# Performance work log

Hardware: AMD Instinct MI355X
Metric: run time of the kernel (lower is better)

The kernel has to match this reference:

```python
import jax, jax.numpy as jnp
import numpy as np

N_HEADS = 16


def setup_inputs() -> dict:
    key = jax.random.key(0)
    k1, k2, k3 = jax.random.split(key, 3)
    B, T, C = 4, 2048, 1024
    x = jax.random.normal(k1, (B, T, C), dtype=jnp.float32)
    # torch nn.Linear weights are (out_features, in_features); y = x @ W.T
    w_in = jax.random.normal(k2, (3 * C, C), dtype=jnp.float32) * 0.02
    w_out = jax.random.normal(k3, (C, C), dtype=jnp.float32) * 0.02
    return {"x": x, "w_in": w_in, "w_out": w_out}


def reference(x, w_in, w_out):
    B, T, C = x.shape
    H = N_HEADS
    hd = C // H

    qkv = x @ w_in.T                      # [B, T, 3C]
    q, k, v = jnp.split(qkv, 3, axis=2)   # each [B, T, C]

    def heads(t):
        return t.reshape(B, T, H, hd).transpose(0, 2, 1, 3)  # [B, H, T, hd]

    q, k, v = heads(q), heads(k), heads(v)

    scale = 1.0 / jnp.sqrt(jnp.float32(hd))
    scores = jnp.einsum('bhqd,bhkd->bhqk', q, k) * scale      # [B, H, T, T]
    causal = jnp.tril(jnp.ones((T, T), dtype=bool))
    scores = jnp.where(causal, scores, -jnp.inf)
    attn = jax.nn.softmax(scores, axis=-1)
    y = jnp.einsum('bhqk,bhkd->bhqd', attn, v)                # [B, H, T, hd]
    y = y.transpose(0, 2, 1, 3).reshape(B, T, C)
    return y @ w_out.T
```

## Files before the change

kernel.cpp:

```cpp
#include <hip/hip_runtime.h>
#include <stdint.h>

#define BB 4
#define TT 2048
#define CC 1024
#define HH 16
#define HD 64
#define C3 3072
#define MM (BB*TT)

typedef __bf16 bf16_t;
typedef bf16_t bf16x8 __attribute__((ext_vector_type(8)));
typedef float f32x4 __attribute__((ext_vector_type(4)));
typedef unsigned short u16;
typedef u16 u16x8 __attribute__((ext_vector_type(8)));
typedef uint32_t u32;

static __device__ __forceinline__ u16 f2bf(float f){
  u32 u = __builtin_bit_cast(u32, f);
  u32 r = (u + 0x7fffu + ((u >> 16) & 1u)) >> 16;
  return (u16)r;
}

static __device__ __forceinline__ f32x4 mfma16(bf16x8 a, bf16x8 b, f32x4 c){
  return __builtin_amdgcn_mfma_f32_16x16x32_bf16(a, b, c, 0, 0, 0);
}

typedef __attribute__((address_space(1))) void* gas_t;
typedef __attribute__((address_space(3))) void* las_t;
static __device__ __forceinline__ void gload16(const void* g, void* l){
  __builtin_amdgcn_global_load_lds((gas_t)g, (las_t)l, 16, 0, 0);
}

__global__ __launch_bounds__(256) void cvt_all(const float* __restrict__ x,
                                               const float* __restrict__ wi,
                                               const float* __restrict__ wo,
                                               u16* __restrict__ out){
  const int n1 = MM*CC/8, n2 = C3*CC/8, n3 = CC*CC/8;
  const int total = n1 + n2 + n3;
  int stride = gridDim.x * blockDim.x;
  for (int i = blockIdx.x * blockDim.x + threadIdx.x; i < total; i += stride){
    const float* src; int k;
    if (i < n1){ src = x; k = i; }
    else if (i < n1 + n2){ src = wi; k = i - n1; }
    else { src = wo; k = i - n1 - n2; }
    const float4* p = (const float4*)src + (size_t)k * 2;
    float4 a = p[0], b = p[1];
    u16x8 o;
    o[0]=f2bf(a.x); o[1]=f2bf(a.y); o[2]=f2bf(a.z); o[3]=f2bf(a.w);
    o[4]=f2bf(b.x); o[5]=f2bf(b.y); o[6]=f2bf(b.z); o[7]=f2bf(b.w);
    *((u16x8*)out + i) = o;
  }
}

template<int OUTBF>
__global__ __launch_bounds__(256) void gemm_bt(const u16* __restrict__ A,
                                               const u16* __restrict__ Bm,
                                               void* __restrict__ Cp,
                                               int M, int N, int K,
                                               int nbx, int cpx){
  __shared__ u16 As[128*64];
  __shared__ u16 Bs[128*64];
  const int bid = blockIdx.x;
  const int nb = (bid & 7) * cpx + (bid >> 3);
  const int by = nb / nbx, bx = nb - by * nbx;
  const int tid  = threadIdx.x;
  const int lane = tid & 63;
  const int w    = tid >> 6;
  const int m0   = by * 128;
  const int n0   = bx * 128;
  const int wm   = (w >> 1) * 64;
  const int wn   = (w & 1) * 64;
  const int lr   = lane & 15;
  const int lg4  = lane >> 4;

  f32x4 acc[4][4] = {};

  const int rq  = tid >> 3;
  const int c8s = ((tid & 7) ^ (rq & 7)) * 8;
  const u16* gA = A  + (size_t)(m0 + rq) * K + c8s;
  const u16* gB = Bm + (size_t)(n0 + rq) * K + c8s;
  char* lA = (char*)As + tid*16;
  char* lB = (char*)Bs + tid*16;

  for (int k0 = 0; k0 < K; k0 += 64){
    #pragma unroll
    for (int q = 0; q < 4; q++){
      gload16(gA + (size_t)(q*32)*K + k0, lA + q*4096);
      gload16(gB + (size_t)(q*32)*K + k0, lB + q*4096);
    }
    __syncthreads();
    #pragma unroll
    for (int kk = 0; kk < 2; kk++){
      bf16x8 af[4], bfr[4];
      #pragma unroll
      for (int m = 0; m < 4; m++){
        int row = wm + m*16 + lr;
        int slot = ((kk<<2) | lg4) ^ (row & 7);
        af[m] = *(const bf16x8*)((const char*)As + row*128 + slot*16);
      }
      #pragma unroll
      for (int n = 0; n < 4; n++){
        int row = wn + n*16 + lr;
        int slot = ((kk<<2) | lg4) ^ (row & 7);
        bfr[n] = *(const bf16x8*)((const char*)Bs + row*128 + slot*16);
      }
      #pragma unroll
      for (int m = 0; m < 4; m++)
        #pragma unroll
        for (int n = 0; n < 4; n++)
          acc[m][n] = mfma16(af[m], bfr[n], acc[m][n]);
    }
    __syncthreads();
  }

  const int cr = lg4 * 4;
  #pragma unroll
  for (int m = 0; m < 4; m++)
    #pragma unroll
    for (int n = 0; n < 4; n++)
      #pragma unroll
      for (int j = 0; j < 4; j++){
        size_t row = (size_t)(m0 + wm + m*16 + cr + j);
        size_t col = (size_t)(n0 + wn + n*16 + lr);
        if (OUTBF) ((u16*)Cp)[row*(size_t)N + col] = f2bf(acc[m][n][j]);
        else       ((float*)Cp)[row*(size_t)N + col] = acc[m][n][j];
      }
}

__global__ __launch_bounds__(256, 3) void attn_fwd(const u16* __restrict__ qkv,
                                                   u16* __restrict__ y){
  __shared__ u16 Kl[2][64*72];
  __shared__ u16 Vt[2][64*72];
  const int bid = blockIdx.x;
  const int tq = bid >> 6;
  const int h = bid & 15, b = (bid >> 4) & 3;
  const int tid = threadIdx.x, lane = tid & 63, w = tid >> 6;
  const int lr = lane & 15, lg = lane >> 4;
  const size_t base = (size_t)b * TT * C3;
  const int qA = tq*64 + w*16;
  const int qB = (31-tq)*64 + w*16;
  const float SC = 0.18033688011112042f;

  bf16x8 qf[2][2];
  {
    const u16* qp0 = qkv + base + (size_t)(qA + lr) * C3 + h*HD;
    qf[0][0] = *(const bf16x8*)(qp0 + lg*8);
    qf[0][1] = *(const bf16x8*)(qp0 + 32 + lg*8);
    const u16* qp1 = qkv + base + (size_t)(qB + lr) * C3 + h*HD;
    qf[1][0] = *(const bf16x8*)(qp1 + lg*8);
    qf[1][1] = *(const bf16x8*)(qp1 + 32 + lg*8);
    #pragma unroll
    for (int m = 0; m < 2; m++)
      #pragma unroll
      for (int i = 0; i < 2; i++)
        #pragma unroll
        for (int e = 0; e < 8; e++)
          qf[m][i][e] = (bf16_t)((float)qf[m][i][e] * SC);
  }

  const int rK = tid >> 3, cK = tid & 7;
  const int rp = tid & 15;
  const int dc = (tid >> 4) & 7;
  const int hf = tid >> 7;
  const u16* gK = qkv + base + (size_t)rK * C3 + CC + h*HD + cK*8;
  const u16* gV = qkv + base + (size_t)(2*rp + 32*hf) * C3 + 2*CC + h*HD + dc*8;

  const int kkey = ((rK >> 3) & 1) << 5;
  const int kw0 = rK*72 + ((cK*8) ^ kkey);
  const int kw1 = (rK+32)*72 + ((cK*8) ^ kkey);
  const int vw  = 2*rp + 32*hf;

  const int rdx = ((lr >> 2) & 1) << 5;
  const int rbase = 8*(lr >> 2) + (lr & 3);

  u16x8 kreg[2], vreg[2];
  kreg[0] = *(const u16x8*)(gK);
  kreg[1] = *(const u16x8*)(gK + (size_t)32*C3);
  vreg[0] = *(const u16x8*)(gV);
  vreg[1] = *(const u16x8*)(gV + C3);

  f32x4 o[2][4] = {};
  float mj[2] = {-1e30f, -1e30f};
  float lj[2] = {0.f, 0.f};

  const int ktmax = 31 - tq;
  for (int kt = 0; kt <= ktmax; kt++){
    const int cb = kt & 1;
    u16* KL = Kl[cb];
    u16* VT = Vt[cb];
    *(u16x8*)&KL[kw0] = kreg[0];
    *(u16x8*)&KL[kw1] = kreg[1];
    #pragma unroll
    for (int e = 0; e < 8; e++){
      u32 pk = (u32)vreg[0][e] | ((u32)vreg[1][e] << 16);
      *(u32*)&VT[(dc*8+e)*72 + vw] = pk;
    }
    __syncthreads();

    if (kt < ktmax){
      const u16* gk2 = gK + (size_t)(kt+1)*64*C3;
      const u16* gv2 = gV + (size_t)(kt+1)*64*C3;
      kreg[0] = *(const u16x8*)(gk2);
      kreg[1] = *(const u16x8*)(gk2 + (size_t)32*C3);
      vreg[0] = *(const u16x8*)(gv2);
      vreg[1] = *(const u16x8*)(gv2 + C3);
    }

    const bool m0act = (kt <= tq);

    #pragma unroll
    for (int m = 1; m >= 0; m--){
      if (m == 0 && !m0act) continue;

      f32x4 s[4] = {};
      __builtin_amdgcn_s_setprio(1);
      #pragma unroll
      for (int n = 0; n < 4; n++){
        const int rho = 32*(n>>1) + 4*(n&1) + rbase;
        bf16x8 kb0 = *(const bf16x8*)&KL[rho*72 + ((     lg*8) ^ rdx)];
        bf16x8 kb1 = *(const bf16x8*)&KL[rho*72 + ((32 + lg*8) ^ rdx)];
        s[n] = mfma16(kb0, qf[m][0], s[n]);
        s[n] = mfma16(kb1, qf[m][1], s[n]);
      }
      __builtin_amdgcn_s_setprio(0);

      const int qrow = (m ? qB : qA) + lr;
      const bool dm = (kt == (m ? ktmax : tq));
      if (dm){
        #pragma unroll
        for (int n = 0; n < 4; n++)
          #pragma unroll
          for (int j = 0; j < 4; j++)
            if (kt*64 + 32*(n>>1) + 8*lg + 4*(n&1) + j > qrow)
              s[n][j] = -1e30f;
      }
      float tm = s[0][0];
      #pragma unroll
      for (int n = 0; n < 4; n++)
        #pragma unroll
        for (int j = 0; j < 4; j++) tm = fmaxf(tm, s[n][j]);
      tm = fmaxf(tm, __shfl_xor(tm, 16, 64));
      tm = fmaxf(tm, __shfl_xor(tm, 32, 64));
      float mo = mj[m];
      if (!__all(tm <= mo + 4.0f)){
        float mn = fmaxf(mo, tm);
        float al = __builtin_amdgcn_exp2f(mo - mn);
        mj[m] = mn;
        lj[m] *= al;
        float a0 = __shfl(al, lg*4+0, 16);
        float a1 = __shfl(al, lg*4+1, 16);
        float a2 = __shfl(al, lg*4+2, 16);
        float a3 = __shfl(al, lg*4+3, 16);
        #pragma unroll
        for (int n = 0; n < 4; n++){
          o[m][n][0] *= a0; o[m][n][1] *= a1;
          o[m][n][2] *= a2; o[m][n][3] *= a3;
        }
      }
      float mm = mj[m];
      float ps = 0.f;
      bf16x8 pa, pb;
      #pragma unroll
      for (int n = 0; n < 4; n++){
        float p0 = __builtin_amdgcn_exp2f(s[n][0] - mm);
        float p1 = __builtin_amdgcn_exp2f(s[n][1] - mm);
        float p2 = __builtin_amdgcn_exp2f(s[n][2] - mm);
        float p3 = __builtin_amdgcn_exp2f(s[n][3] - mm);
        ps += (p0 + p1) + (p2 + p3);
        if (n == 0){ pa[0]=(bf16_t)p0; pa[1]=(bf16_t)p1; pa[2]=(bf16_t)p2; pa[3]=(bf16_t)p3; }
        if (n == 1){ pa[4]=(bf16_t)p0; pa[5]=(bf16_t)p1; pa[6]=(bf16_t)p2; pa[7]=(bf16_t)p3; }
        if (n == 2){ pb[0]=(bf16_t)p0; pb[1]=(bf16_t)p1; pb[2]=(bf16_t)p2; pb[3]=(bf16_t)p3; }
        if (n == 3){ pb[4]=(bf16_t)p0; pb[5]=(bf16_t)p1; pb[6]=(bf16_t)p2; pb[7]=(bf16_t)p3; }
      }
      ps += __shfl_xor(ps, 16, 64);
      ps += __shfl_xor(ps, 32, 64);
      lj[m] += ps;

      __builtin_amdgcn_s_setprio(1);
      #pragma unroll
      for (int n = 0; n < 4; n++){
        bf16x8 vb0 = *(const bf16x8*)&VT[(n*16+lr)*72 +      lg*8];
        bf16x8 vb1 = *(const bf16x8*)&VT[(n*16+lr)*72 + 32 + lg*8];
        o[m][n] = mfma16(pa, vb0, o[m][n]);
        o[m][n] = mfma16(pb, vb1, o[m][n]);
      }
      __builtin_amdgcn_s_setprio(0);
      __builtin_amdgcn_sched_barrier(0);
    }
  }

  #pragma unroll
  for (int m = 0; m < 2; m++){
    float inv = 1.0f / lj[m];
    float i0 = __shfl(inv, lg*4+0, 16);
    float i1 = __shfl(inv, lg*4+1, 16);
    float i2 = __shfl(inv, lg*4+2, 16);
    float i3 = __shfl(inv, lg*4+3, 16);
    const int qb = (m ? qB : qA);
    #pragma unroll
    for (int j = 0; j < 4; j++){
      float ij = (j==0) ? i0 : (j==1) ? i1 : (j==2) ? i2 : i3;
      size_t row = (size_t)b*TT + qb + lg*4 + j;
      #pragma unroll
      for (int n = 0; n < 4; n++)
        y[row*CC + h*HD + n*16 + lr] = f2bf(o[m][n][j] * ij);
    }
  }
}

extern "C" void kernel_launch(void* const* d_in, const int* in_sizes, int n_in,
                              void* d_out, int out_size, void* d_ws, size_t ws_size,
                              hipStream_t stream){
  const float* x     = (const float*)d_in[0];
  const float* w_in  = (const float*)d_in[1];
  const float* w_out = (const float*)d_in[2];
  float* out = (float*)d_out;

  u16* xb   = (u16*)d_ws;
  u16* wib  = xb  + (size_t)MM * CC;
  u16* wob  = wib + (size_t)C3 * CC;
  u16* qkvb = wob + (size_t)CC * CC;
  u16* yb   = xb;

  cvt_all<<<2048, 256, 0, stream>>>(x, w_in, w_out, xb);

  gemm_bt<1><<<1536, 256, 0, stream>>>(xb, wib, (void*)qkvb, MM, C3, CC, 24, 192);
  attn_fwd<<<1024, 256, 0, stream>>>(qkvb, yb);
  gemm_bt<0><<<512, 256, 0, stream>>>(yb, wob, (void*)out, MM, CC, CC, 8, 64);
}
```

Before: 166.9 us.

## Hoist V fragment loads across both query tiles and swizzle V^T smem

Loads the V^T fragments from shared memory once per key tile into registers and reuses them for both query row groups, instead of reloading them for each group. Adds an XOR swizzle on the V^T column index to reduce LDS bank conflicts. Also reshapes the max and sum reductions into trees, removes the sched_barrier, and lowers the launch-bounds occupancy hint from 3 to 2 to make room for the extra registers. The cost is higher register pressure and possibly fewer resident waves per CU.

```diff
diff --git a/kernel.cpp b/kernel.cpp
--- a/kernel.cpp
+++ b/kernel.cpp
@@ -128,7 +128,7 @@
       }
 }
 
-__global__ __launch_bounds__(256, 3) void attn_fwd(const u16* __restrict__ qkv,
+__global__ __launch_bounds__(256, 2) void attn_fwd(const u16* __restrict__ qkv,
                                                    u16* __restrict__ y){
   __shared__ u16 Kl[2][64*72];
   __shared__ u16 Vt[2][64*72];
@@ -169,7 +169,7 @@
   const int kkey = ((rK >> 3) & 1) << 5;
   const int kw0 = rK*72 + ((cK*8) ^ kkey);
   const int kw1 = (rK+32)*72 + ((cK*8) ^ kkey);
-  const int vw  = 2*rp + 32*hf;
+  const int vcol = (2*rp + 32*hf) ^ (8*dc);
 
   const int rdx = ((lr >> 2) & 1) << 5;
   const int rbase = 8*(lr >> 2) + (lr & 3);
@@ -194,7 +194,7 @@
     #pragma unroll
     for (int e = 0; e < 8; e++){
       u32 pk = (u32)vreg[0][e] | ((u32)vreg[1][e] << 16);
-      *(u32*)&VT[(dc*8+e)*72 + vw] = pk;
+      *(u32*)&VT[(dc*8+e)*72 + vcol] = pk;
     }
     __syncthreads();
 
@@ -208,6 +208,7 @@
     }
 
     const bool m0act = (kt <= tq);
+    bf16x8 vb[8];
 
     #pragma unroll
     for (int m = 1; m >= 0; m--){
@@ -225,6 +226,16 @@
       }
       __builtin_amdgcn_s_setprio(0);
 
+      if (m == 1){
+        #pragma unroll
+        for (int n = 0; n < 4; n++){
+          const int dcr = (2*n + (lr >> 3)) & 7;
+          const int c0 = (lg ^ dcr) * 8;
+          vb[2*n]   = *(const bf16x8*)&VT[(n*16+lr)*72 + c0];
+          vb[2*n+1] = *(const bf16x8*)&VT[(n*16+lr)*72 + (c0 ^ 32)];
+        }
+      }
+
       const int qrow = (m ? qB : qA) + lr;
       const bool dm = (kt == (m ? ktmax : tq));
       if (dm){
@@ -235,11 +246,11 @@
             if (kt*64 + 32*(n>>1) + 8*lg + 4*(n&1) + j > qrow)
               s[n][j] = -1e30f;
       }
-      float tm = s[0][0];
-      #pragma unroll
-      for (int n = 0; n < 4; n++)
-        #pragma unroll
-        for (int j = 0; j < 4; j++) tm = fmaxf(tm, s[n][j]);
+      float x0 = fmaxf(fmaxf(s[0][0], s[0][1]), fmaxf(s[0][2], s[0][3]));
+      float x1 = fmaxf(fmaxf(s[1][0], s[1][1]), fmaxf(s[1][2], s[1][3]));
+      float x2 = fmaxf(fmaxf(s[2][0], s[2][1]), fmaxf(s[2][2], s[2][3]));
+      float x3 = fmaxf(fmaxf(s[3][0], s[3][1]), fmaxf(s[3][2], s[3][3]));
+      float tm = fmaxf(fmaxf(x0, x1), fmaxf(x2, x3));
       tm = fmaxf(tm, __shfl_xor(tm, 16, 64));
       tm = fmaxf(tm, __shfl_xor(tm, 32, 64));
       float mo = mj[m];
@@ -259,7 +270,7 @@
         }
       }
       float mm = mj[m];
-      float ps = 0.f;
+      float psn[4];
       bf16x8 pa, pb;
       #pragma unroll
       for (int n = 0; n < 4; n++){
@@ -267,12 +278,13 @@
         float p1 = __builtin_amdgcn_exp2f(s[n][1] - mm);
         float p2 = __builtin_amdgcn_exp2f(s[n][2] - mm);
         float p3 = __builtin_amdgcn_exp2f(s[n][3] - mm);
-        ps += (p0 + p1) + (p2 + p3);
+        psn[n] = (p0 + p1) + (p2 + p3);
         if (n == 0){ pa[0]=(bf16_t)p0; pa[1]=(bf16_t)p1; pa[2]=(bf16_t)p2; pa[3]=(bf16_t)p3; }
         if (n == 1){ pa[4]=(bf16_t)p0; pa[5]=(bf16_t)p1; pa[6]=(bf16_t)p2; pa[7]=(bf16_t)p3; }
         if (n == 2){ pb[0]=(bf16_t)p0; pb[1]=(bf16_t)p1; pb[2]=(bf16_t)p2; pb[3]=(bf16_t)p3; }
         if (n == 3){ pb[4]=(bf16_t)p0; pb[5]=(bf16_t)p1; pb[6]=(bf16_t)p2; pb[7]=(bf16_t)p3; }
       }
+      float ps = (psn[0] + psn[1]) + (psn[2] + psn[3]);
       ps += __shfl_xor(ps, 16, 64);
       ps += __shfl_xor(ps, 32, 64);
       lj[m] += ps;
@@ -280,13 +292,10 @@
       __builtin_amdgcn_s_setprio(1);
       #pragma unroll
       for (int n = 0; n < 4; n++){
-        bf16x8 vb0 = *(const bf16x8*)&VT[(n*16+lr)*72 +      lg*8];
-        bf16x8 vb1 = *(const bf16x8*)&VT[(n*16+lr)*72 + 32 + lg*8];
-        o[m][n] = mfma16(pa, vb0, o[m][n]);
-        o[m][n] = mfma16(pb, vb1, o[m][n]);
+        o[m][n] = mfma16(pa, vb[2*n],   o[m][n]);
+        o[m][n] = mfma16(pb, vb[2*n+1], o[m][n]);
       }
       __builtin_amdgcn_s_setprio(0);
-      __builtin_amdgcn_sched_barrier(0);
     }
   }
 
```

Result: no change. 165.1 us (-1.1%).
